# Kernel tuning notes

Measured on AMD Instinct MI355X. Metric: run time of the kernel, lower is better.

The kernel has to match this reference:

```python
import jax, jax.numpy as jnp
import numpy as np

HIDDEN = 768
ENT = 9
D = 64  # inner_dim
BIG = 1e12


def _rope_tables(seq_len, dim):
    # layout after torch stack([sin,cos],-1).reshape: [sin0,cos0,sin1,cos1,...]
    pos = jnp.arange(seq_len, dtype=jnp.float32)[:, None]          # [S,1]
    inv = jnp.power(10000.0, -2.0 * jnp.arange(dim // 2, dtype=jnp.float32) / dim)
    ang = pos * inv                                                 # [S,D/2]
    # repeat_interleave(2): [c0,c0,c1,c1,...]
    cos = jnp.repeat(jnp.cos(ang), 2, axis=-1)[:, None, :]          # [S,1,D]
    sin = jnp.repeat(jnp.sin(ang), 2, axis=-1)[:, None, :]
    return sin, cos


def _rotate_half_interleaved(x):
    # stack([-x_odd, x_even], -1).reshape -> [-x1, x0, -x3, x2, ...]
    return jnp.stack([-x[..., 1::2], x[..., ::2]], axis=-1).reshape(x.shape)


def _multilabel_ce(logits, labels):
    # standard GlobalPointer multilabel categorical crossentropy
    B = logits.shape[0]
    y_pred = logits.reshape(B * ENT, -1)
    y_true = labels.reshape(B * ENT, -1)
    y_pred = (1.0 - 2.0 * y_true) * y_pred
    y_neg = y_pred - y_true * BIG
    y_pos = y_pred - (1.0 - y_true) * BIG
    neg = jnp.logaddexp(0.0, jax.scipy.special.logsumexp(y_neg, axis=-1))
    pos = jnp.logaddexp(0.0, jax.scipy.special.logsumexp(y_pos, axis=-1))
    return jnp.mean(neg + pos)


def setup_inputs() -> dict:
    key = jax.random.key(0)
    k1, k2, k3, k4 = jax.random.split(key, 4)
    B, S = 16, 512
    last_hidden_state = jax.random.normal(k1, (B, S, HIDDEN), dtype=jnp.float32)
    attention_mask = jnp.ones((B, S), dtype=jnp.int32)
    batch_labels = jax.random.randint(k2, (B, ENT, S, S), 0, 2).astype(jnp.int32)
    W = jax.random.normal(k3, (HIDDEN, ENT * D * 2), dtype=jnp.float32) * 0.02
    b = jnp.zeros((ENT * D * 2,), dtype=jnp.float32)
    return {"last_hidden_state": last_hidden_state, "attention_mask": attention_mask,
            "batch_labels": batch_labels, "W": W, "b": b}


def reference(last_hidden_state, attention_mask, batch_labels, W, b):
    B, S, _ = last_hidden_state.shape
    out = last_hidden_state @ W + b                     # [B,S,ENT*2D]
    out = out.reshape(B, S, ENT, 2 * D)
    qw, kw = out[..., :D], out[..., D:]                 # [B,S,ENT,D]

    sin, cos = _rope_tables(S, D)                       # [S,1,D]
    qw = qw * cos + _rotate_half_interleaved(qw) * sin
    kw = kw * cos + _rotate_half_interleaved(kw) * sin

    logits = jnp.einsum('bmhd,bnhd->bhmn', qw, kw)      # [B,ENT,S,S]

    pad = attention_mask.astype(jnp.float32)[:, None, None, :]  # mask over key dim n
    logits = logits * pad - (1.0 - pad) * BIG
    tril = jnp.tril(jnp.ones((S, S), dtype=jnp.float32), -1)
    logits = logits - tril * BIG
    temp_logits = logits / (D ** 0.5)

    loss = _multilabel_ce(temp_logits, batch_labels.astype(jnp.float32))
    return loss, temp_logits
```

## Files before the change

### kernel.cpp

```cpp
#include <hip/hip_runtime.h>
#include <hip/hip_bf16.h>

#define HID 768
#define ENTS 9
#define DD 64
#define NOUT 1152
#define BATCH 16
#define SEQ 512
#define BIGF 1000000000000.0f
#define BIG8 125000000000.0f
#define NCHUNK 16

typedef __attribute__((ext_vector_type(8))) short short8;
typedef __attribute__((ext_vector_type(4))) short short4_t;
typedef __attribute__((ext_vector_type(4))) float floatx4;
typedef __attribute__((ext_vector_type(2))) float floatx2;
typedef __attribute__((ext_vector_type(4))) int intx4;
typedef unsigned short ushort_t;

static __device__ __forceinline__ ushort_t f2bf(float x) {
    unsigned int u = __float_as_uint(x);
    unsigned int r = (u + 0x7FFFu + ((u >> 16) & 1u)) >> 16;
    return (ushort_t)r;
}

static __device__ __forceinline__ void gload16(const void* g, void* l) {
    __builtin_amdgcn_global_load_lds(
        (const __attribute__((address_space(1))) void*)g,
        (__attribute__((address_space(3))) void*)l, 16, 0, 0);
}

__global__ void rope_table_kernel(float* __restrict__ sin_t, float* __restrict__ cos_t) {
    int idx = blockIdx.x * blockDim.x + threadIdx.x;
    if (idx >= SEQ * 32) return;
    int m = idx >> 5, i = idx & 31;
    float inv = powf(10000.0f, -2.0f * (float)i / 64.0f);
    float ang = (float)m * inv;
    sin_t[idx] = sinf(ang);
    cos_t[idx] = cosf(ang);
}

__global__ void cvt_x_kernel(const float* __restrict__ X, ushort_t* __restrict__ Xb, int n) {
    int i = (blockIdx.x * blockDim.x + threadIdx.x) * 4;
    int stride = gridDim.x * blockDim.x * 4;
    for (; i < n; i += stride) {
        float4 f = *(const float4*)&X[i];
        ushort_t u0 = f2bf(f.x), u1 = f2bf(f.y), u2 = f2bf(f.z), u3 = f2bf(f.w);
        ushort_t* p = &Xb[i];
        p[0] = u0; p[1] = u1; p[2] = u2; p[3] = u3;
    }
}

__global__ void cvt_w_kernel(const float* __restrict__ W, ushort_t* __restrict__ Wt) {
    int idx = blockIdx.x * blockDim.x + threadIdx.x;
    if (idx >= NOUT * HID) return;
    int n = idx / HID, k = idx - n * HID;
    Wt[idx] = f2bf(W[(size_t)k * NOUT + n]);
}

__global__ __launch_bounds__(256) void proj_rope_kernel(
    const ushort_t* __restrict__ Xb, const ushort_t* __restrict__ Wt,
    const float* __restrict__ bias,
    const float* __restrict__ sin_t, const float* __restrict__ cos_t,
    ushort_t* __restrict__ qbuf, ushort_t* __restrict__ kbuf)
{
    __shared__ ushort_t As[128 * 32];
    __shared__ ushort_t Bs[128 * 32];
    const int tid  = threadIdx.x;
    const int lane = tid & 63;
    const int wave = tid >> 6;
    const int bm = blockIdx.x * 128;
    const int bn = blockIdx.y * 128;
    const int wm = (wave >> 1) * 64;
    const int wn = (wave & 1) * 64;

    floatx4 acc[4][4];
    #pragma unroll
    for (int j = 0; j < 4; ++j)
        #pragma unroll
        for (int i = 0; i < 4; ++i) { floatx4 z = {0.f,0.f,0.f,0.f}; acc[j][i] = z; }

    const int c0 = wave * 64 + lane;
    const int c1 = 256 + wave * 64 + lane;
    const int r0 = c0 >> 2, q0 = (c0 & 3) * 8;
    const int r1 = c1 >> 2, q1 = (c1 & 3) * 8;
    ushort_t* ldsA0 = As + wave * 512;
    ushort_t* ldsA1 = As + 2048 + wave * 512;
    ushort_t* ldsB0 = Bs + wave * 512;
    ushort_t* ldsB1 = Bs + 2048 + wave * 512;

    const int ko = (lane >> 4) * 8;
    const int lr = lane & 15;

    for (int kt = 0; kt < HID; kt += 32) {
        gload16(&Xb[(size_t)(bm + r0) * HID + kt + q0], ldsA0);
        gload16(&Xb[(size_t)(bm + r1) * HID + kt + q1], ldsA1);
        gload16(&Wt[(size_t)(bn + r0) * HID + kt + q0], ldsB0);
        gload16(&Wt[(size_t)(bn + r1) * HID + kt + q1], ldsB1);
        __syncthreads();

        short8 a[4], b[4];
        #pragma unroll
        for (int i = 0; i < 4; ++i) a[i] = *(const short8*)&As[(wm + i*16 + lr) * 32 + ko];
        #pragma unroll
        for (int j = 0; j < 4; ++j) b[j] = *(const short8*)&Bs[(wn + j*16 + lr) * 32 + ko];
        #pragma unroll
        for (int j = 0; j < 4; ++j)
            #pragma unroll
            for (int i = 0; i < 4; ++i)
                acc[j][i] = __builtin_amdgcn_mfma_f32_16x16x32_bf16(b[j], a[i], acc[j][i], 0, 0, 0);
        __syncthreads();
    }

    #pragma unroll
    for (int j = 0; j < 4; ++j) {
        const int n0 = bn + wn + j*16 + (lane >> 4) * 4;
        const int e   = n0 >> 7;
        const int dd0 = n0 & 127;
        const bool isq = dd0 < DD;
        const int d0  = isq ? dd0 : dd0 - DD;
        const float4 bv = *(const float4*)&bias[n0];
        #pragma unroll
        for (int i = 0; i < 4; ++i) {
            const int m = bm + wm + i*16 + lr;
            const int s  = m & (SEQ - 1);
            const int bb = m >> 9;
            const float c0f = cos_t[s*32 + (d0 >> 1)];
            const float s0f = sin_t[s*32 + (d0 >> 1)];
            const float c1f = cos_t[s*32 + (d0 >> 1) + 1];
            const float s1f = sin_t[s*32 + (d0 >> 1) + 1];
            const float v0 = acc[j][i][0] + bv.x;
            const float v1 = acc[j][i][1] + bv.y;
            const float v2 = acc[j][i][2] + bv.z;
            const float v3 = acc[j][i][3] + bv.w;
            const float o0 = v0 * c0f - v1 * s0f;
            const float o1 = v1 * c0f + v0 * s0f;
            const float o2 = v2 * c1f - v3 * s1f;
            const float o3 = v3 * c1f + v2 * s1f;
            short4_t sv = { (short)f2bf(o0), (short)f2bf(o1), (short)f2bf(o2), (short)f2bf(o3) };
            size_t oidx = (((size_t)(bb * ENTS + e) * SEQ) + s) * DD + d0;
            *(short4_t*)&(isq ? qbuf : kbuf)[oidx] = sv;
        }
    }
}

__global__ __launch_bounds__(256) void qk_mask_ce_kernel(
    const ushort_t* __restrict__ qbuf, const ushort_t* __restrict__ kbuf,
    const int* __restrict__ amask, const int* __restrict__ labels,
    float* __restrict__ logits, float* __restrict__ partials)
{
    __shared__ ushort_t Qs[128][72];
    __shared__ ushort_t Ks[128][72];
    __shared__ float ssn[4], ssp[4];
    const int tid  = threadIdx.x;
    const int lane = tid & 63;
    const int wave = tid >> 6;
    const int bm = blockIdx.x * 128;
    const int bn = blockIdx.y * 128;
    const int bh = blockIdx.z;
    const int b  = bh / ENTS;
    const int wm = (wave >> 1) * 64;
    const int wn = (wave & 1) * 64;
    const size_t base = (size_t)bh * SEQ * DD;

    const int g  = lane >> 4;
    const int lr = lane & 15;
    const int ko = g * 8;
    const int r0 = bm + wm + lr;
    const int W  = bn + wn;
    const int n00 = W + (g << 2);
    const int bhbase = bh << 18;

    const bool diag = (blockIdx.x == blockIdx.y);
    const float lowAdj = (blockIdx.x > blockIdx.y) ? -BIG8 : 0.0f;

    intx4 y[4][4];
    #pragma unroll
    for (int j = 0; j < 4; ++j)
        #pragma unroll
        for (int i = 0; i < 4; ++i)
            y[j][i] = __builtin_nontemporal_load(
                (const intx4*)&labels[bhbase + ((r0 + i*16) << 9) + n00 + j*16]);

    floatx4 pm8[4], pc[4];
    #pragma unroll
    for (int j = 0; j < 4; ++j) {
        const intx4 p4 = *(const intx4*)&amask[(b << 9) + n00 + j*16];
        #pragma unroll
        for (int rg = 0; rg < 4; ++rg) {
            const float pf = (float)p4[rg];
            pm8[j][rg] = pf * 0.125f;
            pc[j][rg]  = (pf - 1.0f) * BIG8 + lowAdj;
        }
    }

    {
        const int r  = tid >> 1;
        const int ks = (tid & 1) * 32;
        const ushort_t* gq = &qbuf[base + (size_t)(bm + r) * DD + ks];
        const ushort_t* gk = &kbuf[base + (size_t)(bn + r) * DD + ks];
        #pragma unroll
        for (int u = 0; u < 4; ++u) {
            *(short8*)&Qs[r][ks + u*8] = *(const short8*)(gq + u*8);
            *(short8*)&Ks[r][ks + u*8] = *(const short8*)(gk + u*8);
        }
    }
    __syncthreads();

    short8 a[2][4];
    #pragma unroll
    for (int kk = 0; kk < 2; ++kk)
        #pragma unroll
        for (int i = 0; i < 4; ++i)
            a[kk][i] = *(const short8*)&Qs[wm + i*16 + lr][kk*32 + ko];

    float smn = 0.f, smp = 0.f;
    float tl[4];
    float* __restrict__ lgb = logits + bhbase;

    #pragma unroll
    for (int jp = 0; jp < 2; ++jp) {
        const int jA = jp * 2, jB = jp * 2 + 1;

        floatx4 accA[4], accB[4];
        #pragma unroll
        for (int i = 0; i < 4; ++i) { floatx4 z = {0.f,0.f,0.f,0.f}; accA[i] = z; accB[i] = z; }
        #pragma unroll
        for (int kk = 0; kk < 2; ++kk) {
            const short8 bfA = *(const short8*)&Ks[wn + jA*16 + lr][kk*32 + ko];
            const short8 bfB = *(const short8*)&Ks[wn + jB*16 + lr][kk*32 + ko];
            #pragma unroll
            for (int i = 0; i < 4; ++i) {
                accA[i] = __builtin_amdgcn_mfma_f32_16x16x32_bf16(bfA, a[kk][i], accA[i], 0, 0, 0);
                accB[i] = __builtin_amdgcn_mfma_f32_16x16x32_bf16(bfB, a[kk][i], accB[i], 0, 0, 0);
            }
        }

        #pragma unroll
        for (int half = 0; half < 2; ++half) {
            const int j = half ? jB : jA;
            const floatx4 pm = pm8[j], pcj = pc[j];
            const int n0j = W + j*16 + (g << 2);
            #pragma unroll
            for (int i = 0; i < 4; ++i) {
                const int m = r0 + i*16;
                const int d = m - n0j;
                floatx4 v = half ? accB[i] : accA[i];
                const intx4 yv = y[j][i];
                #pragma unroll
                for (int rg = 0; rg < 4; ++rg) {
                    float t = fmaf(v[rg], pm[rg], pcj[rg]);
                    if (diag && (d > rg)) t -= BIG8;
                    v[rg] = t;
                    const int yy = yv[rg] & 1;
                    const float u = __uint_as_float(__float_as_uint(t) ^ ((unsigned)yy << 31));
                    const float cN = yy ? -BIGF : 0.0f;
                    const float cP = yy ? -BIG8 : -BIGF;
                    smn += __expf(u + cN);
                    smp += __expf(u + cP);
                }
                if (half) accB[i] = v; else accA[i] = v;
            }
        }

        #pragma unroll
        for (int i = 0; i < 4; ++i) {
            const floatx4 vA = accA[i], vB = accB[i];
            const int m = r0 + i*16;
            float* __restrict__ row = lgb + (m << 9);
            const float sameA  = __shfl(vA.w, (lane - 16) & 63);
            const float tailA  = __shfl(tl[i], lr + 48);
            const float sameB  = __shfl(vB.w, (lane - 16) & 63);
            const float crossB = __shfl(vA.w, lr + 48);
            const float uA0 = (g == 0) ? tailA  : sameA;
            const float uB0 = (g == 0) ? crossB : sameB;
            if (jp == 0 && g == 0) {
                row[W] = vA.x;
                floatx2 h2 = { vA.y, vA.z };
                *(floatx2*)&row[W + 1] = h2;
            } else {
                floatx4 uA = { uA0, vA.x, vA.y, vA.z };
                *(floatx4*)&row[W + jA*16 + (g << 2) - 1] = uA;
            }
            floatx4 uB = { uB0, vB.x, vB.y, vB.z };
            *(floatx4*)&row[W + jB*16 + (g << 2) - 1] = uB;
            tl[i] = vB.w;
        }
    }

    if (g == 3) {
        #pragma unroll
        for (int i = 0; i < 4; ++i) {
            const int m = r0 + i*16;
            lgb[(m << 9) + W + 63] = tl[i];
        }
    }

    #pragma unroll
    for (int off = 32; off > 0; off >>= 1) {
        smn += __shfl_down(smn, off);
        smp += __shfl_down(smp, off);
    }
    if (lane == 0) { ssn[wave] = smn; ssp[wave] = smp; }
    __syncthreads();
    if (tid == 0) {
        float SN = ssn[0] + ssn[1] + ssn[2] + ssn[3];
        float SP = ssp[0] + ssp[1] + ssp[2] + ssp[3];
        const int chunk = blockIdx.x * 4 + blockIdx.y;
        floatx2 res = { SN, SP };
        *(floatx2*)&partials[(size_t)(bh * NCHUNK + chunk) * 2] = res;
    }
}

static __device__ __forceinline__ float lae0(float x) {
    return fmaxf(x, 0.f) + log1pf(__expf(-fabsf(x)));
}

__global__ __launch_bounds__(256) void ce_final_kernel(
    const float* __restrict__ partials, float* __restrict__ out)
{
    __shared__ float red[256];
    const int t = threadIdx.x;
    float val = 0.f;
    if (t < BATCH * ENTS) {
        float SN = 0.f, SP = 0.f;
        for (int c = 0; c < NCHUNK; ++c) {
            SN += partials[(size_t)(t * NCHUNK + c) * 2];
            SP += partials[(size_t)(t * NCHUNK + c) * 2 + 1];
        }
        const float neg = log1pf(SN);
        const float pos = lae0(BIG8 + logf(SP));
        val = neg + pos;
    }
    red[t] = val;
    __syncthreads();
    for (int s2 = 128; s2 > 0; s2 >>= 1) {
        if (t < s2) red[t] += red[t + s2];
        __syncthreads();
    }
    if (t == 0) out[0] = red[0] / (float)(BATCH * ENTS);
}

extern "C" void kernel_launch(void* const* d_in, const int* in_sizes, int n_in,
                              void* d_out, int out_size, void* d_ws, size_t ws_size,
                              hipStream_t stream) {
    const float* X      = (const float*)d_in[0];
    const int*   amask  = (const int*)d_in[1];
    const int*   labels = (const int*)d_in[2];
    const float* W      = (const float*)d_in[3];
    const float* bias   = (const float*)d_in[4];

    float* out    = (float*)d_out;
    float* logits = out + 1;

    float* sin_t = (float*)d_ws;
    float* cos_t = sin_t + SEQ * 32;
    ushort_t* Xb   = (ushort_t*)(cos_t + SEQ * 32);
    ushort_t* Wt   = Xb + (size_t)BATCH * SEQ * HID;
    ushort_t* qbuf = Wt + (size_t)NOUT * HID;
    ushort_t* kbuf = qbuf + (size_t)BATCH * ENTS * SEQ * DD;
    float* partials = (float*)(kbuf + (size_t)BATCH * ENTS * SEQ * DD);

    rope_table_kernel<<<64, 256, 0, stream>>>(sin_t, cos_t);
    cvt_x_kernel<<<1024, 256, 0, stream>>>(X, Xb, BATCH * SEQ * HID);
    cvt_w_kernel<<<(NOUT * HID + 255) / 256, 256, 0, stream>>>(W, Wt);
    proj_rope_kernel<<<dim3(64, 9), 256, 0, stream>>>(Xb, Wt, bias, sin_t, cos_t, qbuf, kbuf);
    qk_mask_ce_kernel<<<dim3(4, 4, 144), 256, 0, stream>>>(qbuf, kbuf, amask, labels, logits, partials);
    ce_final_kernel<<<1, 256, 0, stream>>>(partials, out);
}
```

Baseline: 154.6 us.

## Skip QK matmul for fully masked lower tiles using a constant fill kernel

The QK/mask/CE kernel now launches only the 4 diagonal and 6 upper 128x128 tiles per batch-head instead of all 16. A new lightweight kernel handles the 6 strictly-lower tiles. Those logits are fixed by the tril and pad masks at float precision, so it writes them as constants and only counts positive labels under valid keys for the CE sums. This removes the Q/K loads, MFMA work and exp evaluations for those tiles, but it relies on the dot product being absorbed by the huge mask constant, and it adds a second launch.

Result: faster. 149.8 us (-3.1%).

```diff
diff --git a/kernel.cpp b/kernel.cpp
--- a/kernel.cpp
+++ b/kernel.cpp
@@ -144,6 +144,62 @@
     }
 }
 
+__global__ __launch_bounds__(256) void lower_fill_kernel(
+    const int* __restrict__ amask, const int* __restrict__ labels,
+    float* __restrict__ logits, float* __restrict__ partials)
+{
+    const int u  = blockIdx.x;
+    const int bh = blockIdx.y;
+    int bx, by;
+    if (u < 3)      { by = 0; bx = u + 1; }
+    else if (u < 5) { by = 1; bx = u - 1; }
+    else            { bx = 3; by = 2; }
+    const int bm = bx * 128, bn = by * 128;
+    const int b  = bh / ENTS;
+    const int bhbase = bh << 18;
+    const int c4 = (threadIdx.x & 31) << 2;
+    const int rr = threadIdx.x >> 5;
+
+    const intx4 pf = *(const intx4*)&amask[(b << 9) + bn + c4];
+    floatx4 cv;
+    #pragma unroll
+    for (int e = 0; e < 4; ++e) cv[e] = (float)pf[e] * BIG8 - 2.0f * BIG8;
+    float cvm1 = 0.f;
+    if (c4 > 0) {
+        const int pfm1 = amask[(b << 9) + bn + c4 - 1];
+        cvm1 = (float)pfm1 * BIG8 - 2.0f * BIG8;
+    }
+    const floatx4 sh = { cvm1, cv.x, cv.y, cv.z };
+    const floatx2 h2 = { cv.y, cv.z };
+
+    int cnt = 0;
+    for (int pass = 0; pass < 16; ++pass) {
+        const int m = bm + pass * 8 + rr;
+        const int off = bhbase + (m << 9) + bn + c4;
+        const intx4 y4 = __builtin_nontemporal_load((const intx4*)&labels[off]);
+        #pragma unroll
+        for (int e = 0; e < 4; ++e) cnt += (y4[e] & 1) & pf[e];
+        if (c4 == 0) {
+            logits[off] = cv.x;
+            *(floatx2*)&logits[off + 1] = h2;
+        } else {
+            *(floatx4*)&logits[off - 1] = sh;
+        }
+        if (c4 == 124) logits[off + 3] = cv.w;
+    }
+
+    #pragma unroll
+    for (int o = 32; o > 0; o >>= 1) cnt += __shfl_down(cnt, o);
+    __shared__ int sred[4];
+    if ((threadIdx.x & 63) == 0) sred[threadIdx.x >> 6] = cnt;
+    __syncthreads();
+    if (threadIdx.x == 0) {
+        float SP = (float)(sred[0] + sred[1] + sred[2] + sred[3]);
+        floatx2 res = { 0.f, SP };
+        *(floatx2*)&partials[(size_t)(bh * NCHUNK + bx * 4 + by) * 2] = res;
+    }
+}
+
 __global__ __launch_bounds__(256) void qk_mask_ce_kernel(
     const ushort_t* __restrict__ qbuf, const ushort_t* __restrict__ kbuf,
     const int* __restrict__ amask, const int* __restrict__ labels,
@@ -155,9 +211,19 @@
     const int tid  = threadIdx.x;
     const int lane = tid & 63;
     const int wave = tid >> 6;
-    const int bm = blockIdx.x * 128;
-    const int bn = blockIdx.y * 128;
-    const int bh = blockIdx.z;
+
+    const int tile = blockIdx.x;
+    const int bh   = blockIdx.y;
+    int bx, by;
+    if (tile < 4) { bx = tile; by = tile; }
+    else {
+        const int t = tile - 4;
+        if (t < 3)      { bx = 0; by = t + 1; }
+        else if (t < 5) { bx = 1; by = t - 1; }
+        else            { bx = 2; by = 3; }
+    }
+    const int bm = bx * 128;
+    const int bn = by * 128;
     const int b  = bh / ENTS;
     const int wm = (wave >> 1) * 64;
     const int wn = (wave & 1) * 64;
@@ -171,8 +237,7 @@
     const int n00 = W + (g << 2);
     const int bhbase = bh << 18;
 
-    const bool diag = (blockIdx.x == blockIdx.y);
-    const float lowAdj = (blockIdx.x > blockIdx.y) ? -BIG8 : 0.0f;
+    const bool diag = (tile < 4);
 
     intx4 y[4][4];
     #pragma unroll
@@ -190,7 +255,7 @@
         for (int rg = 0; rg < 4; ++rg) {
             const float pf = (float)p4[rg];
             pm8[j][rg] = pf * 0.125f;
-            pc[j][rg]  = (pf - 1.0f) * BIG8 + lowAdj;
+            pc[j][rg]  = (pf - 1.0f) * BIG8;
         }
     }
 
@@ -200,9 +265,9 @@
         const ushort_t* gq = &qbuf[base + (size_t)(bm + r) * DD + ks];
         const ushort_t* gk = &kbuf[base + (size_t)(bn + r) * DD + ks];
         #pragma unroll
-        for (int u = 0; u < 4; ++u) {
-            *(short8*)&Qs[r][ks + u*8] = *(const short8*)(gq + u*8);
-            *(short8*)&Ks[r][ks + u*8] = *(const short8*)(gk + u*8);
+        for (int uu = 0; uu < 4; ++uu) {
+            *(short8*)&Qs[r][ks + uu*8] = *(const short8*)(gq + uu*8);
+            *(short8*)&Ks[r][ks + uu*8] = *(const short8*)(gk + uu*8);
         }
     }
     __syncthreads();
@@ -253,11 +318,11 @@
                     if (diag && (d > rg)) t -= BIG8;
                     v[rg] = t;
                     const int yy = yv[rg] & 1;
-                    const float u = __uint_as_float(__float_as_uint(t) ^ ((unsigned)yy << 31));
+                    const float uu = __uint_as_float(__float_as_uint(t) ^ ((unsigned)yy << 31));
                     const float cN = yy ? -BIGF : 0.0f;
                     const float cP = yy ? -BIG8 : -BIGF;
-                    smn += __expf(u + cN);
-                    smp += __expf(u + cP);
+                    smn += __expf(uu + cN);
+                    smp += __expf(uu + cP);
                 }
                 if (half) accB[i] = v; else accA[i] = v;
             }
@@ -306,9 +371,8 @@
     if (tid == 0) {
         float SN = ssn[0] + ssn[1] + ssn[2] + ssn[3];
         float SP = ssp[0] + ssp[1] + ssp[2] + ssp[3];
-        const int chunk = blockIdx.x * 4 + blockIdx.y;
         floatx2 res = { SN, SP };
-        *(floatx2*)&partials[(size_t)(bh * NCHUNK + chunk) * 2] = res;
+        *(floatx2*)&partials[(size_t)(bh * NCHUNK + bx * 4 + by) * 2] = res;
     }
 }
 
@@ -365,6 +429,7 @@
     cvt_x_kernel<<<1024, 256, 0, stream>>>(X, Xb, BATCH * SEQ * HID);
     cvt_w_kernel<<<(NOUT * HID + 255) / 256, 256, 0, stream>>>(W, Wt);
     proj_rope_kernel<<<dim3(64, 9), 256, 0, stream>>>(Xb, Wt, bias, sin_t, cos_t, qbuf, kbuf);
-    qk_mask_ce_kernel<<<dim3(4, 4, 144), 256, 0, stream>>>(qbuf, kbuf, amask, labels, logits, partials);
+    qk_mask_ce_kernel<<<dim3(10, 144), 256, 0, stream>>>(qbuf, kbuf, amask, labels, logits, partials);
+    lower_fill_kernel<<<dim3(6, 144), 256, 0, stream>>>(amask, labels, logits, partials);
     ce_final_kernel<<<1, 256, 0, stream>>>(partials, out);
 }
```
